# Performance work log

Measured on AMD Instinct MI355X. Metric: run time of the kernel, lower is better.

Reference implementation:

```python
import jax, jax.numpy as jnp
import numpy as np

N_HEADS = 32
N_KV_HEADS = 8
HEAD_DIM = 128
DIM = 4096
ROPE_THETA = 500000.0
B, S = 2, 2048


def setup_inputs() -> dict:
    key = jax.random.key(0)
    k1, k2, k3, k4, k5 = jax.random.split(key, 5)
    sd = 0.02
    return {
        "x": jax.random.normal(k1, (B, S, DIM), dtype=jnp.float32),
        "wq": jax.random.normal(k2, (DIM, N_HEADS * HEAD_DIM), dtype=jnp.float32) * sd,
        "wk": jax.random.normal(k3, (DIM, N_KV_HEADS * HEAD_DIM), dtype=jnp.float32) * sd,
        "wv": jax.random.normal(k4, (DIM, N_KV_HEADS * HEAD_DIM), dtype=jnp.float32) * sd,
        "wo": jax.random.normal(k5, (N_HEADS * HEAD_DIM, DIM), dtype=jnp.float32) * sd,
    }


def _rope_freqs(seqlen, head_dim, theta):
    inv = 1.0 / (theta ** (jnp.arange(0, head_dim, 2, dtype=jnp.float32) / head_dim))
    ang = jnp.arange(seqlen, dtype=jnp.float32)[:, None] * inv[None, :]  # [S, hd/2]
    return jnp.cos(ang), jnp.sin(ang)


def _apply_rope(t, cos, sin):
    # t: [B, S, H, hd]; complex multiply on interleaved (even, odd) pairs
    tr = t.reshape(*t.shape[:-1], HEAD_DIM // 2, 2)
    a, b = tr[..., 0], tr[..., 1]
    c = cos[None, :, None, :]
    s = sin[None, :, None, :]
    out = jnp.stack([a * c - b * s, a * s + b * c], axis=-1)
    return out.reshape(t.shape)


def reference(x, wq, wk, wv, wo):
    bsz, seqlen, _ = x.shape
    n_rep = N_HEADS // N_KV_HEADS
    q = (x @ wq).reshape(bsz, seqlen, N_HEADS, HEAD_DIM)
    k = (x @ wk).reshape(bsz, seqlen, N_KV_HEADS, HEAD_DIM)
    v = (x @ wv).reshape(bsz, seqlen, N_KV_HEADS, HEAD_DIM)

    cos, sin = _rope_freqs(seqlen, HEAD_DIM, ROPE_THETA)
    q = _apply_rope(q, cos, sin)
    k = _apply_rope(k, cos, sin)

    # repeat_kv: expand kv heads to n_heads (torch.repeat_interleave dim=2)
    k = jnp.repeat(k, n_rep, axis=2)  # [B, S, H, hd]
    v = jnp.repeat(v, n_rep, axis=2)

    scale = 1.0 / jnp.sqrt(jnp.float32(HEAD_DIM))
    scores = jnp.einsum("bqhd,bkhd->bhqk", q, k) * scale  # [B, H, S, S]
    causal = jnp.tril(jnp.ones((seqlen, seqlen), dtype=bool))
    scores = jnp.where(causal[None, None], scores, jnp.float32(-1e9))
    probs = jax.nn.softmax(scores, axis=-1)
    out = jnp.einsum("bhqk,bkhd->bqhd", probs, v)  # [B, S, H, hd]
    out = out.reshape(bsz, seqlen, N_HEADS * HEAD_DIM)
    return out @ wo
```

## Files before the change

kernel.cpp:

```cpp
#include <hip/hip_runtime.h>
#include <stdint.h>

typedef unsigned short u16;
using short8 = __attribute__((ext_vector_type(8))) short;
using f32x4  = __attribute__((ext_vector_type(4))) float;

#define S_LEN 2048
#define NH 32
#define NKV 8
#define HD 128
#define DIM 4096
#define NQ 4096
#define NKVD 1024

typedef __attribute__((address_space(1))) unsigned int uGLB;
typedef __attribute__((address_space(3))) unsigned int uLDS;

__device__ __forceinline__ void g2l16(const u16* g, u16* l) {
  __builtin_amdgcn_global_load_lds((const uGLB*)g, (uLDS*)l, 16, 0, 0);
}

__device__ __forceinline__ float b2f(u16 u) {
  union { unsigned u32; float f; } x; x.u32 = ((unsigned)u) << 16; return x.f;
}
__device__ __forceinline__ u16 f2b(float f) {
  union { float f; unsigned u32; } x; x.f = f;
  unsigned lsb = (x.u32 >> 16) & 1u;
  x.u32 += 0x7fffu + lsb;
  return (u16)(x.u32 >> 16);
}

__global__ __launch_bounds__(256) void transpose_cast(const float* __restrict__ in,
                                                      u16* __restrict__ out,
                                                      int K, int N) {
  __shared__ float tile[32][33];
  int n0 = blockIdx.x * 32, k0 = blockIdx.y * 32;
  int tx = threadIdx.x, ty = threadIdx.y;
#pragma unroll
  for (int j = 0; j < 4; ++j)
    tile[ty + j * 8][tx] = in[(size_t)(k0 + ty + j * 8) * N + n0 + tx];
  __syncthreads();
#pragma unroll
  for (int j = 0; j < 4; ++j)
    out[(size_t)(n0 + ty + j * 8) * K + k0 + tx] = f2b(tile[tx][ty + j * 8]);
}

__global__ __launch_bounds__(256) void cast_x(const float* __restrict__ in,
                                              u16* __restrict__ out, int n4) {
  int i = blockIdx.x * 256 + threadIdx.x;
  if (i >= n4) return;
  float4 v = reinterpret_cast<const float4*>(in)[i];
  ushort4 u;
  u.x = f2b(v.x); u.y = f2b(v.y); u.z = f2b(v.z); u.w = f2b(v.w);
  reinterpret_cast<ushort4*>(out)[i] = u;
}

__global__ __launch_bounds__(512) void gemm256(const u16* __restrict__ A,
                                               const u16* __restrict__ Bt,
                                               int N, int mode,
                                               float* __restrict__ out,
                                               u16* __restrict__ Qb,
                                               u16* __restrict__ Kb,
                                               u16* __restrict__ Vt) {
  const int K = 4096;
  const int NT = 64;
  __shared__ __align__(16) u16 lds[2][2][2][8192];

  int tid  = threadIdx.x;
  int lane = tid & 63, w = tid >> 6;
  int ml   = lane & 15, quad = lane >> 4;
  int wm   = w >> 2, wn = w & 3;

  int nwg = gridDim.x * gridDim.y;
  int bid = blockIdx.y * gridDim.x + blockIdx.x;
  int sbid = (bid & 7) * (nwg >> 3) + (bid >> 3);
  int bx = sbid % gridDim.x, by = sbid / gridDim.x;
  int m0 = by * 256, n0 = bx * 256;

  int dst  = w * 1024 + lane * 16;
  int lg   = dst ^ (((lane >> 5) & 1) << 5);
  int srow = lg >> 7, scol = (lg & 127) >> 1;
  const u16* pA = A  + (size_t)(m0 + srow) * K + scol;
  const u16* pB = Bt + (size_t)(n0 + srow) * K + scol;

#define STAGE(mat, T, hh) do { \
    int _b = (T) & 1; \
    int _Tc = (T) < NT ? (T) : (NT - 1); \
    const u16* _s = ((mat) ? pB : pA) + (size_t)(hh) * 128 * K + (size_t)_Tc * 64; \
    u16* _d = &lds[_b][mat][hh][w * 512]; \
    g2l16(_s, _d); \
    g2l16(_s + (size_t)64 * K, _d + 4096); \
  } while (0)

  f32x4 acc[8][4] = {};
  int rxor = ((ml >> 2) & 1) << 5;
  int aoff = ml * 128 + ((quad * 16) ^ rxor);
  int boff = (wn & 1) * 8192 + aoff;

  STAGE(0, 0, 0); STAGE(0, 0, 1); STAGE(1, 0, 0); STAGE(1, 0, 1);
  STAGE(0, 1, 0);
  asm volatile("s_waitcnt vmcnt(2)" ::: "memory");
  __builtin_amdgcn_s_barrier();

  short8 af[4][2], bf0[2][2], bf1[2][2];

  for (int t = 0; t < NT; ++t) {
    int buf = t & 1;
    const char* Ab = reinterpret_cast<const char*>(&lds[buf][0][wm][0]);
    const char* Bb = reinterpret_cast<const char*>(&lds[buf][1][wn >> 1][0]);

#pragma unroll
    for (int mi = 0; mi < 4; ++mi)
#pragma unroll
      for (int ks = 0; ks < 2; ++ks)
        af[mi][ks] = *reinterpret_cast<const short8*>(Ab + aoff + mi * 2048 + ks * 64);
#pragma unroll
    for (int ni = 0; ni < 2; ++ni)
#pragma unroll
      for (int ks = 0; ks < 2; ++ks)
        bf0[ni][ks] = *reinterpret_cast<const short8*>(Bb + boff + ni * 2048 + ks * 64);
    STAGE(0, t + 1, 1);
    __builtin_amdgcn_s_barrier();
    asm volatile("s_waitcnt lgkmcnt(0)" ::: "memory");
    __builtin_amdgcn_sched_barrier(0);
    __builtin_amdgcn_s_setprio(1);
#pragma unroll
    for (int mi = 0; mi < 4; ++mi)
#pragma unroll
      for (int ni = 0; ni < 2; ++ni)
#pragma unroll
        for (int ks = 0; ks < 2; ++ks)
          acc[mi][ni] = __builtin_amdgcn_mfma_f32_16x16x32_bf16(af[mi][ks], bf0[ni][ks], acc[mi][ni], 0, 0, 0);
    __builtin_amdgcn_s_setprio(0);
    __builtin_amdgcn_s_barrier();

#pragma unroll
    for (int ni = 0; ni < 2; ++ni)
#pragma unroll
      for (int ks = 0; ks < 2; ++ks)
        bf1[ni][ks] = *reinterpret_cast<const short8*>(Bb + boff + (2 + ni) * 2048 + ks * 64);
    STAGE(1, t + 1, 0);
    __builtin_amdgcn_s_barrier();
    asm volatile("s_waitcnt lgkmcnt(0)" ::: "memory");
    __builtin_amdgcn_sched_barrier(0);
    __builtin_amdgcn_s_setprio(1);
#pragma unroll
    for (int mi = 0; mi < 4; ++mi)
#pragma unroll
      for (int ni = 0; ni < 2; ++ni)
#pragma unroll
        for (int ks = 0; ks < 2; ++ks)
          acc[mi][2 + ni] = __builtin_amdgcn_mfma_f32_16x16x32_bf16(af[mi][ks], bf1[ni][ks], acc[mi][2 + ni], 0, 0, 0);
    __builtin_amdgcn_s_setprio(0);
    __builtin_amdgcn_s_barrier();

#pragma unroll
    for (int mi = 0; mi < 4; ++mi)
#pragma unroll
      for (int ks = 0; ks < 2; ++ks)
        af[mi][ks] = *reinterpret_cast<const short8*>(Ab + aoff + 8192 + mi * 2048 + ks * 64);
    STAGE(1, t + 1, 1);
    __builtin_amdgcn_s_barrier();
    asm volatile("s_waitcnt lgkmcnt(0)" ::: "memory");
    __builtin_amdgcn_sched_barrier(0);
    __builtin_amdgcn_s_setprio(1);
#pragma unroll
    for (int mi = 0; mi < 4; ++mi)
#pragma unroll
      for (int ni = 0; ni < 2; ++ni)
#pragma unroll
        for (int ks = 0; ks < 2; ++ks)
          acc[4 + mi][ni] = __builtin_amdgcn_mfma_f32_16x16x32_bf16(af[mi][ks], bf0[ni][ks], acc[4 + mi][ni], 0, 0, 0);
    __builtin_amdgcn_s_setprio(0);
    __builtin_amdgcn_s_barrier();

    STAGE(0, t + 2, 0);
    __builtin_amdgcn_s_barrier();
    __builtin_amdgcn_s_setprio(1);
#pragma unroll
    for (int mi = 0; mi < 4; ++mi)
#pragma unroll
      for (int ni = 0; ni < 2; ++ni)
#pragma unroll
        for (int ks = 0; ks < 2; ++ks)
          acc[4 + mi][2 + ni] = __builtin_amdgcn_mfma_f32_16x16x32_bf16(af[mi][ks], bf1[ni][ks], acc[4 + mi][2 + ni], 0, 0, 0);
    __builtin_amdgcn_s_setprio(0);
    asm volatile("s_waitcnt vmcnt(2)" ::: "memory");
    __builtin_amdgcn_s_barrier();
  }
#undef STAGE

#pragma unroll
  for (int mi = 0; mi < 8; ++mi) {
#pragma unroll
    for (int ni = 0; ni < 4; ++ni) {
#pragma unroll
      for (int r = 0; r < 4; ++r) {
        int row = m0 + wm * 128 + mi * 16 + quad * 4 + r;
        int col = n0 + wn * 64 + ni * 16 + ml;
        float v = acc[mi][ni][r];
        if (mode == 1) {
          out[(size_t)row * N + col] = v;
        } else {
          int b = row >> 11, s = row & (S_LEN - 1);
          if (col < NQ) {
            int h = col >> 7, d = col & 127;
            Qb[((size_t)((b * NH + h) * S_LEN + s)) * HD + d] = f2b(v);
          } else if (col < NQ + NKVD) {
            int cc = col - NQ; int h = cc >> 7, d = cc & 127;
            Kb[((size_t)((b * NKV + h) * S_LEN + s)) * HD + d] = f2b(v);
          } else {
            int cc = col - NQ - NKVD; int h = cc >> 7, d = cc & 127;
            Vt[((size_t)((b * NKV + h) * HD + d)) * S_LEN + s] = f2b(v);
          }
        }
      }
    }
  }
}

__global__ __launch_bounds__(256) void rope_ip(u16* __restrict__ X, int npairs) {
  int idx = blockIdx.x * 256 + threadIdx.x;
  if (idx >= npairs) return;
  int i = idx & 63;
  int s = (idx >> 6) & (S_LEN - 1);
  float inv = __expf(-0.2050369278939421f * (float)i);
  float ang = (float)s * inv;
  float sn, cs;
  sincosf(ang, &sn, &cs);
  ushort2 pr = reinterpret_cast<ushort2*>(X)[idx];
  float a = b2f(pr.x), b = b2f(pr.y);
  ushort2 o;
  o.x = f2b(a * cs - b * sn);
  o.y = f2b(a * sn + b * cs);
  reinterpret_cast<ushort2*>(X)[idx] = o;
}

__global__ __launch_bounds__(256, 3) void flash(const u16* __restrict__ Qb,
                                                const u16* __restrict__ Kb,
                                                const u16* __restrict__ Vt,
                                                u16* __restrict__ AO) {
  __shared__ __align__(16) u16 Ks[64 * 128];
  __shared__ __align__(16) u16 Vs[128 * 64];
  __shared__ __align__(16) u16 Ps[4 * 16 * 80];

  int tid  = threadIdx.x;
  int lane = tid & 63, w = tid >> 6;
  int ml   = lane & 15, quad = lane >> 4;
  int q_tile = blockIdx.x, h = blockIdx.y, b = blockIdx.z;
  int hkv = h >> 2;
  int q0  = q_tile * 64;
  const u16* Qh = Qb + ((size_t)(b * NH + h) * S_LEN) * HD;
  const u16* Kh = Kb + ((size_t)(b * NKV + hkv) * S_LEN) * HD;
  const u16* Vh = Vt + ((size_t)(b * NKV + hkv) * HD) * S_LEN;
  u16* Pw = Ps + w * 16 * 80;

  short8 qf[4];
#pragma unroll
  for (int ks = 0; ks < 4; ++ks)
    qf[ks] = *reinterpret_cast<const short8*>(
        Qh + (size_t)(q0 + w * 16 + ml) * HD + ks * 32 + quad * 8);

  short8 ones8;
  {
    u16 one_b = 0x3f80;
#pragma unroll
    for (int j = 0; j < 8; ++j) ones8[j] = (short)one_b;
  }

  f32x4 o[8] = {};
  f32x4 o9 = {};
  const float SC = 0.12751745f;
  const float BIAS = 18.0f;

  int qg = q0 + w * 16 + ml;
  int ntile = q_tile + 1;
  for (int it = 0; it < ntile; ++it) {
    int kv0 = it * 64;
    __syncthreads();
#pragma unroll
    for (int p = 0; p < 4; ++p) {
      int slot = w * 256 + p * 64 + lane;
      int krow = slot >> 4, kch = slot & 15;
      int ksrc = kch ^ (krow & 15);
      g2l16(Kh + (size_t)(kv0 + krow) * HD + ksrc * 8, &Ks[(w * 256 + p * 64) * 8]);
      int vrow = slot >> 3, vch = slot & 7;
      int vsrc = vch ^ (vrow & 7);
      g2l16(Vh + (size_t)vrow * S_LEN + kv0 + vsrc * 8, &Vs[(w * 256 + p * 64) * 8]);
    }
    __syncthreads();

    f32x4 st[4] = {};
#pragma unroll
    for (int ks = 0; ks < 4; ++ks) {
#pragma unroll
      for (int nt = 0; nt < 4; ++nt) {
        int row = nt * 16 + ml;
        int ch = ((ks << 2) | quad) ^ ml;
        short8 kf = *reinterpret_cast<const short8*>(&Ks[row * 128 + ch * 8]);
        st[nt] = __builtin_amdgcn_mfma_f32_16x16x32_bf16(kf, qf[ks], st[nt], 0, 0, 0);
      }
    }

    bool diag = (it == q_tile);
#pragma unroll
    for (int nt = 0; nt < 4; ++nt) {
      float p0 = exp2f(fmaf(st[nt][0], SC, -BIAS));
      float p1 = exp2f(fmaf(st[nt][1], SC, -BIAS));
      float p2 = exp2f(fmaf(st[nt][2], SC, -BIAS));
      float p3 = exp2f(fmaf(st[nt][3], SC, -BIAS));
      if (diag) {
        int kg = kv0 + nt * 16 + quad * 4;
        if (kg + 0 > qg) p0 = 0.f;
        if (kg + 1 > qg) p1 = 0.f;
        if (kg + 2 > qg) p2 = 0.f;
        if (kg + 3 > qg) p3 = 0.f;
      }
      uint2 pk;
      pk.x = (unsigned)f2b(p0) | ((unsigned)f2b(p1) << 16);
      pk.y = (unsigned)f2b(p2) | ((unsigned)f2b(p3) << 16);
      *reinterpret_cast<uint2*>(&Pw[ml * 80 + nt * 16 + quad * 4]) = pk;
    }

#pragma unroll
    for (int ks2 = 0; ks2 < 2; ++ks2) {
      short8 pf = *reinterpret_cast<const short8*>(&Pw[ml * 80 + ks2 * 32 + quad * 8]);
#pragma unroll
      for (int dt = 0; dt < 8; ++dt) {
        int row = dt * 16 + ml;
        int ch = ((ks2 << 2) | quad) ^ (ml & 7);
        short8 vf = *reinterpret_cast<const short8*>(&Vs[row * 64 + ch * 8]);
        o[dt] = __builtin_amdgcn_mfma_f32_16x16x32_bf16(pf, vf, o[dt], 0, 0, 0);
      }
      o9 = __builtin_amdgcn_mfma_f32_16x16x32_bf16(pf, ones8, o9, 0, 0, 0);
    }
  }

  size_t row_base = (size_t)(b * S_LEN + q0 + w * 16 + quad * 4);
#pragma unroll
  for (int r = 0; r < 4; ++r) {
    float inv_l = 1.0f / o9[r];
#pragma unroll
    for (int dt = 0; dt < 8; ++dt) {
      int col = h * HD + dt * 16 + ml;
      AO[(row_base + r) * (size_t)DIM + col] = f2b(o[dt][r] * inv_l);
    }
  }
}

extern "C" void kernel_launch(void* const* d_in, const int* in_sizes, int n_in,
                              void* d_out, int out_size, void* d_ws, size_t ws_size,
                              hipStream_t stream) {
  const float* x  = (const float*)d_in[0];
  const float* wq = (const float*)d_in[1];
  const float* wk = (const float*)d_in[2];
  const float* wv = (const float*)d_in[3];
  const float* wo = (const float*)d_in[4];
  float* out = (float*)d_out;
  char* ws = (char*)d_ws;

  u16* Wqt = (u16*)(ws + 0);
  u16* Wkt = (u16*)(ws + 33554432);
  u16* Wvt = (u16*)(ws + 41943040);
  u16* Xb  = (u16*)(ws + 50331648);
  u16* Qb  = (u16*)(ws + 83886080);
  u16* Kb  = (u16*)(ws + 117440512);
  u16* Vt  = (u16*)(ws + 125829120);

  transpose_cast<<<dim3(128, 128), dim3(32, 8), 0, stream>>>(wq, Wqt, 4096, 4096);
  transpose_cast<<<dim3(32, 128),  dim3(32, 8), 0, stream>>>(wk, Wkt, 4096, 1024);
  transpose_cast<<<dim3(32, 128),  dim3(32, 8), 0, stream>>>(wv, Wvt, 4096, 1024);
  cast_x<<<16384, 256, 0, stream>>>(x, Xb, 4194304);

  gemm256<<<dim3(24, 16), 512, 0, stream>>>(Xb, Wqt, 6144, 0, nullptr, Qb, Kb, Vt);

  rope_ip<<<32768, 256, 0, stream>>>(Qb, 8388608);
  rope_ip<<<8192, 256, 0, stream>>>(Kb, 2097152);

  transpose_cast<<<dim3(128, 128), dim3(32, 8), 0, stream>>>(wo, Wqt, 4096, 4096);

  flash<<<dim3(32, 32, 2), 256, 0, stream>>>(Qb, Kb, Vt, Xb);

  gemm256<<<dim3(16, 16), 512, 0, stream>>>(Xb, Wqt, 4096, 1, out, nullptr, nullptr, nullptr);
}
```

Baseline: 850.6 us.

## Add 128x256-tile QKV GEMM kernel and switch LDS swizzle to full XOR

Adds a dedicated gemm128 kernel for the fused QKV projection that uses 128x256 tiles, launching 768 workgroups instead of 384 for better CU coverage on the 6144-wide projection. It has its own staging schedule that prefetches B two steps ahead. The LDS layout swizzle changes in both GEMMs from a single-bit XOR to an XOR of the 16-byte chunk index with the row, aiming to cut LDS bank conflicts on the fragment reads. The output GEMM drops its mode branch. Smaller tiles lower per-block arithmetic intensity and use more LDS (96 KB), which may limit occupancy.

```diff
diff --git a/kernel.cpp b/kernel.cpp
--- a/kernel.cpp
+++ b/kernel.cpp
@@ -57,11 +57,8 @@
 
 __global__ __launch_bounds__(512) void gemm256(const u16* __restrict__ A,
                                                const u16* __restrict__ Bt,
-                                               int N, int mode,
-                                               float* __restrict__ out,
-                                               u16* __restrict__ Qb,
-                                               u16* __restrict__ Kb,
-                                               u16* __restrict__ Vt) {
+                                               int N,
+                                               float* __restrict__ out) {
   const int K = 4096;
   const int NT = 64;
   __shared__ __align__(16) u16 lds[2][2][2][8192];
@@ -77,11 +74,11 @@
   int bx = sbid % gridDim.x, by = sbid / gridDim.x;
   int m0 = by * 256, n0 = bx * 256;
 
-  int dst  = w * 1024 + lane * 16;
-  int lg   = dst ^ (((lane >> 5) & 1) << 5);
-  int srow = lg >> 7, scol = (lg & 127) >> 1;
-  const u16* pA = A  + (size_t)(m0 + srow) * K + scol;
-  const u16* pB = Bt + (size_t)(n0 + srow) * K + scol;
+  int dstB = w * 1024 + lane * 16;
+  int r    = dstB >> 7;
+  int cg   = ((dstB >> 4) & 7) ^ (r & 7);
+  const u16* pA = A  + (size_t)(m0 + r) * K + cg * 8;
+  const u16* pB = Bt + (size_t)(n0 + r) * K + cg * 8;
 
 #define STAGE(mat, T, hh) do { \
     int _b = (T) & 1; \
@@ -93,8 +90,8 @@
   } while (0)
 
   f32x4 acc[8][4] = {};
-  int rxor = ((ml >> 2) & 1) << 5;
-  int aoff = ml * 128 + ((quad * 16) ^ rxor);
+  int cxa  = (quad ^ (ml & 7)) << 4;
+  int aoff = ml * 128 + cxa;
   int boff = (wn & 1) * 8192 + aoff;
 
   STAGE(0, 0, 0); STAGE(0, 0, 1); STAGE(1, 0, 0); STAGE(1, 0, 1);
@@ -113,12 +110,12 @@
     for (int mi = 0; mi < 4; ++mi)
 #pragma unroll
       for (int ks = 0; ks < 2; ++ks)
-        af[mi][ks] = *reinterpret_cast<const short8*>(Ab + aoff + mi * 2048 + ks * 64);
+        af[mi][ks] = *reinterpret_cast<const short8*>(Ab + (aoff ^ (ks << 6)) + mi * 2048);
 #pragma unroll
     for (int ni = 0; ni < 2; ++ni)
 #pragma unroll
       for (int ks = 0; ks < 2; ++ks)
-        bf0[ni][ks] = *reinterpret_cast<const short8*>(Bb + boff + ni * 2048 + ks * 64);
+        bf0[ni][ks] = *reinterpret_cast<const short8*>(Bb + (boff ^ (ks << 6)) + ni * 2048);
     STAGE(0, t + 1, 1);
     __builtin_amdgcn_s_barrier();
     asm volatile("s_waitcnt lgkmcnt(0)" ::: "memory");
@@ -138,7 +135,7 @@
     for (int ni = 0; ni < 2; ++ni)
 #pragma unroll
       for (int ks = 0; ks < 2; ++ks)
-        bf1[ni][ks] = *reinterpret_cast<const short8*>(Bb + boff + (2 + ni) * 2048 + ks * 64);
+        bf1[ni][ks] = *reinterpret_cast<const short8*>(Bb + (boff ^ (ks << 6)) + (2 + ni) * 2048);
     STAGE(1, t + 1, 0);
     __builtin_amdgcn_s_barrier();
     asm volatile("s_waitcnt lgkmcnt(0)" ::: "memory");
@@ -158,7 +155,7 @@
     for (int mi = 0; mi < 4; ++mi)
 #pragma unroll
       for (int ks = 0; ks < 2; ++ks)
-        af[mi][ks] = *reinterpret_cast<const short8*>(Ab + aoff + 8192 + mi * 2048 + ks * 64);
+        af[mi][ks] = *reinterpret_cast<const short8*>(Ab + 8192 + (aoff ^ (ks << 6)) + mi * 2048);
     STAGE(1, t + 1, 1);
     __builtin_amdgcn_s_barrier();
     asm volatile("s_waitcnt lgkmcnt(0)" ::: "memory");
@@ -195,24 +192,139 @@
 #pragma unroll
     for (int ni = 0; ni < 4; ++ni) {
 #pragma unroll
-      for (int r = 0; r < 4; ++r) {
-        int row = m0 + wm * 128 + mi * 16 + quad * 4 + r;
+      for (int rr = 0; rr < 4; ++rr) {
+        int row = m0 + wm * 128 + mi * 16 + quad * 4 + rr;
         int col = n0 + wn * 64 + ni * 16 + ml;
-        float v = acc[mi][ni][r];
-        if (mode == 1) {
-          out[(size_t)row * N + col] = v;
+        out[(size_t)row * N + col] = acc[mi][ni][rr];
+      }
+    }
+  }
+}
+
+__global__ __launch_bounds__(512) void gemm128(const u16* __restrict__ A,
+                                               const u16* __restrict__ Bt,
+                                               u16* __restrict__ Qb,
+                                               u16* __restrict__ Kb,
+                                               u16* __restrict__ Vt) {
+  const int K = 4096;
+  const int NT = 64;
+  __shared__ __align__(16) char L[98304];
+
+  int tid  = threadIdx.x;
+  int lane = tid & 63, w = tid >> 6;
+  int ml   = lane & 15, quad = lane >> 4;
+  int wm   = w >> 2, wn = w & 3;
+
+  int nwg = gridDim.x * gridDim.y;
+  int bid = blockIdx.y * gridDim.x + blockIdx.x;
+  int sbid = (bid & 7) * (nwg >> 3) + (bid >> 3);
+  int bx = sbid % gridDim.x, by = sbid / gridDim.x;
+  int m0 = by * 128, n0 = bx * 256;
+
+  int dstB = w * 1024 + lane * 16;
+  int r    = dstB >> 7;
+  int cg   = ((dstB >> 4) & 7) ^ (r & 7);
+  const u16* pA = A  + (size_t)(m0 + r) * K + cg * 8;
+  const u16* pB = Bt + (size_t)(n0 + r) * K + cg * 8;
+
+#define STAGE_A(T, h) do { \
+    int _b = (T) & 1; int _Tc = (T) < NT ? (T) : (NT - 1); \
+    g2l16(pA + (size_t)(h) * 64 * K + (size_t)_Tc * 64, \
+          (u16*)(L + _b * 16384 + (h) * 8192 + w * 1024)); \
+  } while (0)
+#define STAGE_B(T, h) do { \
+    int _b = (T) & 1; int _Tc = (T) < NT ? (T) : (NT - 1); \
+    const u16* _s = pB + (size_t)(h) * 128 * K + (size_t)_Tc * 64; \
+    char* _d = L + 32768 + _b * 32768 + (h) * 16384 + w * 1024; \
+    g2l16(_s, (u16*)_d); \
+    g2l16(_s + (size_t)64 * K, (u16*)(_d + 8192)); \
+  } while (0)
+
+  f32x4 acc[4][4] = {};
+  int cxa  = (quad ^ (ml & 7)) << 4;
+  int aoff = ml * 128 + cxa;
+  int boff = (wn & 1) * 8192 + aoff;
+
+  STAGE_A(0, 0); STAGE_A(0, 1); STAGE_B(0, 0); STAGE_B(0, 1);
+  STAGE_B(1, 0); STAGE_B(1, 1);
+  asm volatile("s_waitcnt vmcnt(4)" ::: "memory");
+  __builtin_amdgcn_s_barrier();
+
+  short8 af[2][2], af2[2][2], bf[4][2];
+
+  for (int t = 0; t < NT; ++t) {
+    int buf = t & 1;
+    const char* Ab = L + buf * 16384 + wm * 8192;
+    const char* Bb = L + 32768 + buf * 32768 + (wn >> 1) * 16384;
+
+#pragma unroll
+    for (int mi = 0; mi < 2; ++mi)
+#pragma unroll
+      for (int ks = 0; ks < 2; ++ks)
+        af[mi][ks] = *reinterpret_cast<const short8*>(Ab + (aoff ^ (ks << 6)) + mi * 2048);
+#pragma unroll
+    for (int ni = 0; ni < 4; ++ni)
+#pragma unroll
+      for (int ks = 0; ks < 2; ++ks)
+        bf[ni][ks] = *reinterpret_cast<const short8*>(Bb + (boff ^ (ks << 6)) + ni * 2048);
+    STAGE_A(t + 1, 0); STAGE_A(t + 1, 1);
+    __builtin_amdgcn_s_barrier();
+    asm volatile("s_waitcnt lgkmcnt(0)" ::: "memory");
+    __builtin_amdgcn_sched_barrier(0);
+    __builtin_amdgcn_s_setprio(1);
+#pragma unroll
+    for (int mi = 0; mi < 2; ++mi)
+#pragma unroll
+      for (int ni = 0; ni < 4; ++ni)
+#pragma unroll
+        for (int ks = 0; ks < 2; ++ks)
+          acc[mi][ni] = __builtin_amdgcn_mfma_f32_16x16x32_bf16(af[mi][ks], bf[ni][ks], acc[mi][ni], 0, 0, 0);
+    __builtin_amdgcn_s_setprio(0);
+    __builtin_amdgcn_s_barrier();
+
+#pragma unroll
+    for (int mi = 0; mi < 2; ++mi)
+#pragma unroll
+      for (int ks = 0; ks < 2; ++ks)
+        af2[mi][ks] = *reinterpret_cast<const short8*>(Ab + 4096 + (aoff ^ (ks << 6)) + mi * 2048);
+    STAGE_B(t + 2, 0); STAGE_B(t + 2, 1);
+    __builtin_amdgcn_s_barrier();
+    asm volatile("s_waitcnt lgkmcnt(0)" ::: "memory");
+    __builtin_amdgcn_sched_barrier(0);
+    __builtin_amdgcn_s_setprio(1);
+#pragma unroll
+    for (int mi = 0; mi < 2; ++mi)
+#pragma unroll
+      for (int ni = 0; ni < 4; ++ni)
+#pragma unroll
+        for (int ks = 0; ks < 2; ++ks)
+          acc[2 + mi][ni] = __builtin_amdgcn_mfma_f32_16x16x32_bf16(af2[mi][ks], bf[ni][ks], acc[2 + mi][ni], 0, 0, 0);
+    __builtin_amdgcn_s_setprio(0);
+    asm volatile("s_waitcnt vmcnt(4)" ::: "memory");
+    __builtin_amdgcn_s_barrier();
+  }
+#undef STAGE_A
+#undef STAGE_B
+
+#pragma unroll
+  for (int a = 0; a < 4; ++a) {
+#pragma unroll
+    for (int ni = 0; ni < 4; ++ni) {
+#pragma unroll
+      for (int rr = 0; rr < 4; ++rr) {
+        int row = m0 + wm * 64 + a * 16 + quad * 4 + rr;
+        int col = n0 + wn * 64 + ni * 16 + ml;
+        float v = acc[a][ni][rr];
+        int b = row >> 11, s = row & (S_LEN - 1);
+        if (col < NQ) {
+          int h = col >> 7, d = col & 127;
+          Qb[((size_t)((b * NH + h) * S_LEN + s)) * HD + d] = f2b(v);
+        } else if (col < NQ + NKVD) {
+          int cc = col - NQ; int h = cc >> 7, d = cc & 127;
+          Kb[((size_t)((b * NKV + h) * S_LEN + s)) * HD + d] = f2b(v);
         } else {
-          int b = row >> 11, s = row & (S_LEN - 1);
-          if (col < NQ) {
-            int h = col >> 7, d = col & 127;
-            Qb[((size_t)((b * NH + h) * S_LEN + s)) * HD + d] = f2b(v);
-          } else if (col < NQ + NKVD) {
-            int cc = col - NQ; int h = cc >> 7, d = cc & 127;
-            Kb[((size_t)((b * NKV + h) * S_LEN + s)) * HD + d] = f2b(v);
-          } else {
-            int cc = col - NQ - NKVD; int h = cc >> 7, d = cc & 127;
-            Vt[((size_t)((b * NKV + h) * HD + d)) * S_LEN + s] = f2b(v);
-          }
+          int cc = col - NQ - NKVD; int h = cc >> 7, d = cc & 127;
+          Vt[((size_t)((b * NKV + h) * HD + d)) * S_LEN + s] = f2b(v);
         }
       }
     }
@@ -338,12 +450,12 @@
 
   size_t row_base = (size_t)(b * S_LEN + q0 + w * 16 + quad * 4);
 #pragma unroll
-  for (int r = 0; r < 4; ++r) {
-    float inv_l = 1.0f / o9[r];
+  for (int rr = 0; rr < 4; ++rr) {
+    float inv_l = 1.0f / o9[rr];
 #pragma unroll
     for (int dt = 0; dt < 8; ++dt) {
       int col = h * HD + dt * 16 + ml;
-      AO[(row_base + r) * (size_t)DIM + col] = f2b(o[dt][r] * inv_l);
+      AO[(row_base + rr) * (size_t)DIM + col] = f2b(o[dt][rr] * inv_l);
     }
   }
 }
@@ -372,7 +484,7 @@
   transpose_cast<<<dim3(32, 128),  dim3(32, 8), 0, stream>>>(wv, Wvt, 4096, 1024);
   cast_x<<<16384, 256, 0, stream>>>(x, Xb, 4194304);
 
-  gemm256<<<dim3(24, 16), 512, 0, stream>>>(Xb, Wqt, 6144, 0, nullptr, Qb, Kb, Vt);
+  gemm128<<<dim3(24, 32), 512, 0, stream>>>(Xb, Wqt, Qb, Kb, Vt);
 
   rope_ip<<<32768, 256, 0, stream>>>(Qb, 8388608);
   rope_ip<<<8192, 256, 0, stream>>>(Kb, 2097152);
@@ -381,5 +493,5 @@
 
   flash<<<dim3(32, 32, 2), 256, 0, stream>>>(Qb, Kb, Vt, Xb);
 
-  gemm256<<<dim3(16, 16), 512, 0, stream>>>(Xb, Wqt, 4096, 1, out, nullptr, nullptr, nullptr);
-}
+  gemm256<<<dim3(16, 16), 512, 0, stream>>>(Xb, Wqt, 4096, out);
+}
```

Result: faster. 823.0 us (-3.2%).
